# Optimization experiments

Hardware: AMD Instinct MI355X
Metric: run time of the kernel (lower is better)

## Reference

```python
import jax, jax.numpy as jnp
import numpy as np

B, CH, IMG, P = 16, 3, 384, 16
D, HEADS, DH, MLP, DEPTH = 384, 6, 64, 1536, 6
INNER = HEADS * DH
PD = P * P * 5 * CH          # SPT patch dim = 3840
GRID = IMG // P              # 24
NP = GRID * GRID             # 576 patches
SEQ = NP + 1                 # +cls = 577


def layer_norm(x, g, b, eps=1e-5):
    mu = jnp.mean(x, axis=-1, keepdims=True)
    var = jnp.var(x, axis=-1, keepdims=True)
    return (x - mu) * jax.lax.rsqrt(var + eps) * g + b


def spt_shifts(x):
    # F.pad semantics: (left,right,top,bottom) with negative = crop
    s1 = jnp.pad(x, ((0, 0), (0, 0), (0, 0), (1, 0)))[:, :, :, :-1]  # (1,-1,0,0)
    s2 = jnp.pad(x, ((0, 0), (0, 0), (0, 0), (0, 1)))[:, :, :, 1:]   # (-1,1,0,0)
    s3 = jnp.pad(x, ((0, 0), (0, 0), (1, 0), (0, 0)))[:, :, :-1, :]  # (0,0,1,-1)
    s4 = jnp.pad(x, ((0, 0), (0, 0), (0, 1), (0, 0)))[:, :, 1:, :]   # (0,0,-1,1)
    return jnp.concatenate([x, s1, s2, s3, s4], axis=1)  # [b, 5c, H, W]


def patchify(x):
    # 'b c (h p1) (w p2) -> b (h w) (p1 p2 c)'
    b, c, _, _ = x.shape
    x = x.reshape(b, c, GRID, P, GRID, P)
    x = x.transpose(0, 2, 4, 3, 5, 1)  # b h w p1 p2 c
    return x.reshape(b, GRID * GRID, P * P * c)


def setup_inputs():
    key = jax.random.key(0)
    ks = jax.random.split(key, 16)
    img = jax.random.normal(ks[0], (B, CH, IMG, IMG), jnp.float32)
    spt_g = jnp.ones((PD,), jnp.float32)
    spt_b = jnp.zeros((PD,), jnp.float32)
    spt_w = jax.random.normal(ks[1], (PD, D), jnp.float32) * (1.0 / np.sqrt(PD))
    spt_bias = jnp.zeros((D,), jnp.float32)
    pos = jax.random.normal(ks[2], (1, SEQ, D), jnp.float32) * 0.02
    cls = jax.random.normal(ks[3], (1, 1, D), jnp.float32) * 0.02
    attn_g = jnp.ones((DEPTH, D), jnp.float32)
    attn_b = jnp.zeros((DEPTH, D), jnp.float32)
    temp = jnp.full((DEPTH,), np.log(DH ** -0.5), jnp.float32)
    wqkv = jax.random.normal(ks[4], (DEPTH, D, 3 * INNER), jnp.float32) * 0.02
    wout = jax.random.normal(ks[5], (DEPTH, INNER, D), jnp.float32) * 0.02
    bout = jnp.zeros((DEPTH, D), jnp.float32)
    ff_g = jnp.ones((DEPTH, D), jnp.float32)
    ff_b = jnp.zeros((DEPTH, D), jnp.float32)
    w1 = jax.random.normal(ks[6], (DEPTH, D, MLP), jnp.float32) * 0.02
    b1 = jnp.zeros((DEPTH, MLP), jnp.float32)
    w2 = jax.random.normal(ks[7], (DEPTH, MLP, D), jnp.float32) * 0.02
    b2 = jnp.zeros((DEPTH, D), jnp.float32)
    return {"img": img, "spt_g": spt_g, "spt_b": spt_b, "spt_w": spt_w,
            "spt_bias": spt_bias, "pos": pos, "cls": cls, "attn_g": attn_g,
            "attn_b": attn_b, "temp": temp, "wqkv": wqkv, "wout": wout,
            "bout": bout, "ff_g": ff_g, "ff_b": ff_b, "w1": w1, "b1": b1,
            "w2": w2, "b2": b2}


def vit_forward(img, spt_g, spt_b, spt_w, spt_bias, pos, cls, attn_g, attn_b,
                temp, wqkv, wout, bout, ff_g, ff_b, w1, b1, w2, b2):
    # SPT patch embedding
    x = patchify(spt_shifts(img))                      # [b, NP, PD]
    x = layer_norm(x, spt_g, spt_b) @ spt_w + spt_bias  # [b, NP, D]
    b = x.shape[0]
    cls_tok = jnp.broadcast_to(cls, (b, 1, D))
    x = jnp.concatenate([cls_tok, x], axis=1) + pos[:, :SEQ]

    eye = jnp.eye(SEQ, dtype=bool)
    neg = -jnp.finfo(x.dtype).max

    def block(x, p):
        ag, ab, t, wq, wo, bo, fg, fb, W1, B1, W2, B2 = p
        h = layer_norm(x, ag, ab)
        qkv = h @ wq                                   # [b, n, 3*inner]
        q, k, v = jnp.split(qkv, 3, axis=-1)
        q = q.reshape(b, SEQ, HEADS, DH).transpose(0, 2, 1, 3)
        k = k.reshape(b, SEQ, HEADS, DH).transpose(0, 2, 1, 3)
        v = v.reshape(b, SEQ, HEADS, DH).transpose(0, 2, 1, 3)
        dots = jnp.einsum('bhid,bhjd->bhij', q, k) * jnp.exp(t)
        dots = jnp.where(eye, neg, dots)               # diagonal mask (LSA)
        attn = jax.nn.softmax(dots, axis=-1)
        out = jnp.einsum('bhij,bhjd->bhid', attn, v)
        out = out.transpose(0, 2, 1, 3).reshape(b, SEQ, INNER)
        x = out @ wo + bo + x
        h = layer_norm(x, fg, fb)
        x = jax.nn.gelu(h @ W1 + B1, approximate=False) @ W2 + B2 + x
        return x, None

    params = (attn_g, attn_b, temp, wqkv, wout, bout, ff_g, ff_b, w1, b1, w2, b2)
    x, _ = jax.lax.scan(block, x, params)
    return x


def reference(img, spt_g, spt_b, spt_w, spt_bias, pos, cls, attn_g, attn_b,
              temp, wqkv, wout, bout, ff_g, ff_b, w1, b1, w2, b2):
    return vit_forward(img, spt_g, spt_b, spt_w, spt_bias, pos, cls, attn_g,
                       attn_b, temp, wqkv, wout, bout, ff_g, ff_b, w1, b1,
                       w2, b2)
```

## Files before the change

kernel.cpp:

```cpp
#include <hip/hip_runtime.h>

typedef unsigned short ushort_t;
typedef __bf16 bf16x8 __attribute__((ext_vector_type(8)));
typedef float f32x4 __attribute__((ext_vector_type(4)));

#define SEQ_ 577
#define D_ 384
#define NTOK (16 * 577)

enum { M_QKV = 0, M_OUT, M_MLP1, M_MLP2 };

__device__ inline float b2f(ushort_t u) {
    unsigned int x = ((unsigned int)u) << 16;
    float f; __builtin_memcpy(&f, &x, 4); return f;
}
__device__ inline ushort_t f2b(float f) {
    unsigned int x; __builtin_memcpy(&x, &f, 4);
    x = x + 0x7fffu + ((x >> 16) & 1u);
    return (ushort_t)(x >> 16);
}

__device__ void transpose_tile(const float* __restrict__ src,
                               ushort_t* __restrict__ dst,
                               int ldn, int ldk, int k0, int n0)
{
    __shared__ float t[64][65];
    const int tid = threadIdx.x;
    const int c = tid & 63, rr = tid >> 6;
#pragma unroll
    for (int i = 0; i < 16; i++) {
        int kl = rr + i * 4;
        t[kl][c] = src[(size_t)(k0 + kl) * ldn + n0 + c];
    }
    __syncthreads();
#pragma unroll
    for (int i = 0; i < 16; i++) {
        int nl = rr + i * 4;
        dst[(size_t)(n0 + nl) * ldk + k0 + c] = f2b(t[c][nl]);
    }
}

__global__ __launch_bounds__(256) void prep_spt_kernel(
    const float* __restrict__ w, ushort_t* __restrict__ wt)
{
    transpose_tile(w, wt, 384, 3840, blockIdx.x * 64, blockIdx.y * 64);
}

__global__ __launch_bounds__(256) void prep_all_kernel(
    const float* __restrict__ wqkv, const float* __restrict__ wout,
    const float* __restrict__ w1, const float* __restrict__ w2,
    ushort_t* __restrict__ W6)
{
    int id = blockIdx.x;
    int l = id / 432;
    int r = id - l * 432;
    ushort_t* qkv_t  = W6 + (size_t)l * 1769472;
    ushort_t* wout_t = qkv_t + 442368;
    ushort_t* w1_t   = wout_t + 147456;
    ushort_t* w2_t   = w1_t + 589824;
    const float* wq = wqkv + (size_t)l * 442368;
    const float* wo = wout + (size_t)l * 147456;
    const float* W1 = w1 + (size_t)l * 589824;
    const float* W2 = w2 + (size_t)l * 589824;
    if (r < 108) {
        int kt = r / 18, nt = r % 18;
        transpose_tile(wq, qkv_t, 1152, 384, kt * 64, nt * 64);
    } else if (r < 144) {
        r -= 108; int kt = r / 6, nt = r % 6;
        transpose_tile(wo, wout_t, 384, 384, kt * 64, nt * 64);
    } else if (r < 288) {
        r -= 144; int kt = r / 24, nt = r % 24;
        transpose_tile(W1, w1_t, 1536, 384, kt * 64, nt * 64);
    } else {
        r -= 288; int kt = r / 6, nt = r % 6;
        transpose_tile(W2, w2_t, 384, 1536, kt * 64, nt * 64);
    }
}

template <int MODE>
__global__ __launch_bounds__(256) void gemm64(
    const ushort_t* __restrict__ A, const ushort_t* __restrict__ Bt,
    ushort_t* __restrict__ Co, float* __restrict__ resid,
    const float* __restrict__ bias,
    int M, int K, int ldc)
{
    __shared__ __align__(16) ushort_t As[2][64][40];
    __shared__ __align__(16) ushort_t Bs[2][64][40];

    const int gx = gridDim.x;
    const int nwg = gx * gridDim.y;
    const int f = blockIdx.y * gx + blockIdx.x;
    const int q = nwg >> 3, rr_ = nwg & 7;
    const int xcd = f & 7, ii = f >> 3;
    const int swz = (xcd < rr_ ? xcd * (q + 1) : rr_ * (q + 1) + (xcd - rr_) * q) + ii;
    const int bx = swz % gx, by = swz / gx;

    const int tid = threadIdx.x;
    const int rowBase = by * 64;
    const int colBase = bx * 64;
    const int nk = K >> 5;
    const int lr = tid >> 2, lk = (tid & 3) * 8;
    const int wv = tid >> 6, lane = tid & 63;
    const int wm = (wv >> 1) * 32, wn = (wv & 1) * 32;
    const int m16 = lane & 15, q4 = lane >> 4, kb = q4 * 8;

    const ushort_t* pa = A + (size_t)(rowBase + lr) * K + lk;
    const ushort_t* pb = Bt + (size_t)(colBase + lr) * K + lk;

    f32x4 acc[2][2];
#pragma unroll
    for (int i = 0; i < 2; i++)
#pragma unroll
        for (int j = 0; j < 2; j++) acc[i][j] = (f32x4){0.f, 0.f, 0.f, 0.f};

    uint4 Ua, Ub, Va, Vb;
    auto gloadU = [&](int kt) {
        Ua = *(const uint4*)(pa + kt * 32);
        Ub = *(const uint4*)(pb + kt * 32);
    };
    auto gloadV = [&](int kt) {
        Va = *(const uint4*)(pa + kt * 32);
        Vb = *(const uint4*)(pb + kt * 32);
    };
    auto swriteU = [&](int buf) {
        *(uint4*)&As[buf][lr][lk] = Ua;
        *(uint4*)&Bs[buf][lr][lk] = Ub;
    };
    auto swriteV = [&](int buf) {
        *(uint4*)&As[buf][lr][lk] = Va;
        *(uint4*)&Bs[buf][lr][lk] = Vb;
    };
    auto compute = [&](int buf) {
        bf16x8 a0 = *(const bf16x8*)&As[buf][wm + m16][kb];
        bf16x8 a1 = *(const bf16x8*)&As[buf][wm + 16 + m16][kb];
        bf16x8 b0 = *(const bf16x8*)&Bs[buf][wn + m16][kb];
        bf16x8 b1 = *(const bf16x8*)&Bs[buf][wn + 16 + m16][kb];
        acc[0][0] = __builtin_amdgcn_mfma_f32_16x16x32_bf16(a0, b0, acc[0][0], 0, 0, 0);
        acc[0][1] = __builtin_amdgcn_mfma_f32_16x16x32_bf16(a0, b1, acc[0][1], 0, 0, 0);
        acc[1][0] = __builtin_amdgcn_mfma_f32_16x16x32_bf16(a1, b0, acc[1][0], 0, 0, 0);
        acc[1][1] = __builtin_amdgcn_mfma_f32_16x16x32_bf16(a1, b1, acc[1][1], 0, 0, 0);
    };

    gloadU(0);
    swriteU(0);
    gloadU(1);
    gloadV(2);
    __syncthreads();

    for (int kt = 0; kt < nk; kt += 2) {
        swriteU(1);
        if (kt + 3 < nk) gloadU(kt + 3);
        compute(0);
        __syncthreads();
        if (kt + 2 < nk) {
            swriteV(0);
            if (kt + 4 < nk) gloadV(kt + 4);
        }
        compute(1);
        __syncthreads();
    }

#pragma unroll
    for (int im = 0; im < 2; im++)
#pragma unroll
        for (int in = 0; in < 2; in++) {
            int col = colBase + wn + in * 16 + m16;
#pragma unroll
            for (int r = 0; r < 4; r++) {
                int row = rowBase + wm + im * 16 + q4 * 4 + r;
                if (row >= M) continue;
                float v = acc[im][in][r];
                if (MODE == M_QKV) {
                    Co[(size_t)row * ldc + col] = f2b(v);
                } else if (MODE == M_MLP1) {
                    float t = v + bias[col];
                    float u = t * (0.7978845608f + 0.0356774081f * t * t);
                    float e = __builtin_amdgcn_exp2f(2.885390082f * u);
                    float gl = t - t * __builtin_amdgcn_rcpf(e + 1.0f);
                    Co[(size_t)row * ldc + col] = f2b(gl);
                } else {
                    size_t o = (size_t)row * ldc + col;
                    resid[o] = resid[o] + v + bias[col];
                }
            }
        }
}

__global__ __launch_bounds__(256) void gemm64_spt_split(
    const ushort_t* __restrict__ A, const ushort_t* __restrict__ Bt,
    float* __restrict__ resid, int rowOff)
{
    __shared__ __align__(16) ushort_t As[2][64][40];
    __shared__ __align__(16) ushort_t Bs[2][64][40];

    const int f = blockIdx.z * 288 + blockIdx.y * 6 + blockIdx.x;
    const int swz = (f & 7) * 144 + (f >> 3);
    const int bz = swz / 288;
    const int rem = swz - bz * 288;
    const int by = rem / 6, bx = rem - by * 6;

    const int K = 3840, nk = 30;
    const int rowBase = by * 64;
    const int colBase = bx * 64;
    const int kbase = bz * 960;

    const int tid = threadIdx.x;
    const int lr = tid >> 2, lk = (tid & 3) * 8;
    const int wv = tid >> 6, lane = tid & 63;
    const int wm = (wv >> 1) * 32, wn = (wv & 1) * 32;
    const int m16 = lane & 15, q4 = lane >> 4, kb = q4 * 8;

    const ushort_t* pa = A + (size_t)(rowBase + lr) * K + kbase + lk;
    const ushort_t* pb = Bt + (size_t)(colBase + lr) * K + kbase + lk;

    f32x4 acc[2][2];
#pragma unroll
    for (int i = 0; i < 2; i++)
#pragma unroll
        for (int j = 0; j < 2; j++) acc[i][j] = (f32x4){0.f, 0.f, 0.f, 0.f};

    uint4 Ua, Ub, Va, Vb;
    auto gloadU = [&](int kt) {
        Ua = *(const uint4*)(pa + kt * 32);
        Ub = *(const uint4*)(pb + kt * 32);
    };
    auto gloadV = [&](int kt) {
        Va = *(const uint4*)(pa + kt * 32);
        Vb = *(const uint4*)(pb + kt * 32);
    };
    auto swriteU = [&](int buf) {
        *(uint4*)&As[buf][lr][lk] = Ua;
        *(uint4*)&Bs[buf][lr][lk] = Ub;
    };
    auto swriteV = [&](int buf) {
        *(uint4*)&As[buf][lr][lk] = Va;
        *(uint4*)&Bs[buf][lr][lk] = Vb;
    };
    auto compute = [&](int buf) {
        bf16x8 a0 = *(const bf16x8*)&As[buf][wm + m16][kb];
        bf16x8 a1 = *(const bf16x8*)&As[buf][wm + 16 + m16][kb];
        bf16x8 b0 = *(const bf16x8*)&Bs[buf][wn + m16][kb];
        bf16x8 b1 = *(const bf16x8*)&Bs[buf][wn + 16 + m16][kb];
        acc[0][0] = __builtin_amdgcn_mfma_f32_16x16x32_bf16(a0, b0, acc[0][0], 0, 0, 0);
        acc[0][1] = __builtin_amdgcn_mfma_f32_16x16x32_bf16(a0, b1, acc[0][1], 0, 0, 0);
        acc[1][0] = __builtin_amdgcn_mfma_f32_16x16x32_bf16(a1, b0, acc[1][0], 0, 0, 0);
        acc[1][1] = __builtin_amdgcn_mfma_f32_16x16x32_bf16(a1, b1, acc[1][1], 0, 0, 0);
    };

    gloadU(0);
    swriteU(0);
    gloadU(1);
    gloadV(2);
    __syncthreads();

    for (int kt = 0; kt < nk; kt += 2) {
        swriteU(1);
        if (kt + 3 < nk) gloadU(kt + 3);
        compute(0);
        __syncthreads();
        if (kt + 2 < nk) {
            swriteV(0);
            if (kt + 4 < nk) gloadV(kt + 4);
        }
        compute(1);
        __syncthreads();
    }

#pragma unroll
    for (int im = 0; im < 2; im++)
#pragma unroll
        for (int in = 0; in < 2; in++) {
            int col = colBase + wn + in * 16 + m16;
#pragma unroll
            for (int r = 0; r < 4; r++) {
                int row = rowBase + wm + im * 16 + q4 * 4 + r;
                int grow = rowOff + row;
                int bb = grow / 576, p = grow - bb * 576;
                size_t o = ((size_t)(bb * SEQ_ + 1 + p)) * D_ + col;
                atomicAdd(&resid[o], acc[im][in][r]);
            }
        }
}

__global__ __launch_bounds__(256) void attn_kernel(
    const ushort_t* __restrict__ qkv, ushort_t* __restrict__ attn,
    const float* __restrict__ temp, int layer)
{
    const int qt = blockIdx.x;
    const int bh = blockIdx.y;
    const int b = bh / 6, hd = bh - b * 6;
    const int tid = threadIdx.x;
    const int wv = tid >> 6, lane = tid & 63;
    const int m16 = lane & 15, q4 = lane >> 4;
    const float sc2 = expf(temp[layer]) * 1.44269504f;

    __shared__ __align__(16) ushort_t Ks[64][72];
    __shared__ __align__(16) ushort_t Vt[64][72];
    __shared__ __align__(16) ushort_t Pw[4][16][72];

    const int qrow = qt * 64 + wv * 16 + m16;
    const int qtok = qrow < SEQ_ ? qrow : SEQ_ - 1;
    const ushort_t* qb = qkv + ((size_t)(b * SEQ_ + qtok)) * 1152 + hd * 64;
    bf16x8 qf0 = *(const bf16x8*)(qb + q4 * 8);
    bf16x8 qf1 = *(const bf16x8*)(qb + 32 + q4 * 8);

    f32x4 accO[4];
#pragma unroll
    for (int dt = 0; dt < 4; dt++) accO[dt] = (f32x4){0.f, 0.f, 0.f, 0.f};
    float l_r[4] = {0.f, 0.f, 0.f, 0.f};

    const int skey = tid >> 2;
    const int scol = (tid & 3) * 16;
    const int vp   = tid & 31;
    const int vdh  = (tid >> 5) * 8;

    for (int kt = 0; kt < 10; kt++) {
        int key = kt * 64 + skey;
        int gkey = key < SEQ_ ? key : 0;
        const ushort_t* kb_ = qkv + ((size_t)(b * SEQ_ + gkey)) * 1152 + 384 + hd * 64;
        uint4 kv0 = *(const uint4*)(kb_ + scol);
        uint4 kv1 = *(const uint4*)(kb_ + scol + 8);
        if (key >= SEQ_) { kv0 = (uint4){0, 0, 0, 0}; kv1 = kv0; }
        int vk0 = kt * 64 + 2 * vp;
        int t0 = vk0 < SEQ_ ? vk0 : 0;
        int t1 = vk0 + 1 < SEQ_ ? vk0 + 1 : 0;
        uint4 va = *(const uint4*)(qkv + ((size_t)(b * SEQ_ + t0)) * 1152 + 768 + hd * 64 + vdh);
        uint4 vb2 = *(const uint4*)(qkv + ((size_t)(b * SEQ_ + t1)) * 1152 + 768 + hd * 64 + vdh);
        if (vk0 >= SEQ_) va = (uint4){0, 0, 0, 0};
        if (vk0 + 1 >= SEQ_) vb2 = (uint4){0, 0, 0, 0};
        __syncthreads();
        *(uint4*)&Ks[skey][scol] = kv0;
        *(uint4*)&Ks[skey][scol + 8] = kv1;
        {
            const ushort_t* e0 = (const ushort_t*)&va;
            const ushort_t* e1 = (const ushort_t*)&vb2;
#pragma unroll
            for (int j = 0; j < 8; j++) {
                unsigned int pack = (unsigned int)e0[j] | ((unsigned int)e1[j] << 16);
                *(unsigned int*)&Vt[vdh + j][2 * vp] = pack;
            }
        }
        __syncthreads();

        f32x4 s[4];
#pragma unroll
        for (int ct = 0; ct < 4; ct++) {
            bf16x8 b0 = *(const bf16x8*)&Ks[ct * 16 + m16][q4 * 8];
            bf16x8 b1 = *(const bf16x8*)&Ks[ct * 16 + m16][32 + q4 * 8];
            f32x4 z = (f32x4){0.f, 0.f, 0.f, 0.f};
            z = __builtin_amdgcn_mfma_f32_16x16x32_bf16(qf0, b0, z, 0, 0, 0);
            z = __builtin_amdgcn_mfma_f32_16x16x32_bf16(qf1, b1, z, 0, 0, 0);
            s[ct] = z;
        }
        const int rowb = qt * 64 + wv * 16 + q4 * 4;
#pragma unroll
        for (int r = 0; r < 4; r++) {
            float rs = 0.f;
#pragma unroll
            for (int ct = 0; ct < 4; ct++) {
                int col = kt * 64 + ct * 16 + m16;
                float v = s[ct][r] * sc2;
                if (col >= SEQ_ || col == rowb + r) v = -1.0e30f;
                float p = __builtin_amdgcn_exp2f(v);
                s[ct][r] = p;
                rs += p;
            }
            rs += __shfl_xor(rs, 1);
            rs += __shfl_xor(rs, 2);
            rs += __shfl_xor(rs, 4);
            rs += __shfl_xor(rs, 8);
            l_r[r] += rs;
        }
#pragma unroll
        for (int ct = 0; ct < 4; ct++)
#pragma unroll
            for (int r = 0; r < 4; r++)
                Pw[wv][q4 * 4 + r][ct * 16 + m16] = f2b(s[ct][r]);
        bf16x8 pf0 = *(const bf16x8*)&Pw[wv][m16][q4 * 8];
        bf16x8 pf1 = *(const bf16x8*)&Pw[wv][m16][32 + q4 * 8];
#pragma unroll
        for (int dt = 0; dt < 4; dt++) {
            bf16x8 vb0 = *(const bf16x8*)&Vt[dt * 16 + m16][q4 * 8];
            bf16x8 vb1 = *(const bf16x8*)&Vt[dt * 16 + m16][32 + q4 * 8];
            f32x4 o = accO[dt];
            o = __builtin_amdgcn_mfma_f32_16x16x32_bf16(pf0, vb0, o, 0, 0, 0);
            o = __builtin_amdgcn_mfma_f32_16x16x32_bf16(pf1, vb1, o, 0, 0, 0);
            accO[dt] = o;
        }
    }

    const int rowb = qt * 64 + wv * 16 + q4 * 4;
#pragma unroll
    for (int r = 0; r < 4; r++) {
        int grow = rowb + r;
        if (grow >= SEQ_) continue;
        float inv = 1.f / l_r[r];
        ushort_t* op = attn + ((size_t)(b * SEQ_ + grow)) * 384 + hd * 64;
#pragma unroll
        for (int dt = 0; dt < 4; dt++)
            op[dt * 16 + m16] = f2b(accO[dt][r] * inv);
    }
}

__global__ __launch_bounds__(256) void spt_ln_kernel(
    const float* __restrict__ img, const float* __restrict__ gg,
    const float* __restrict__ bb_, ushort_t* __restrict__ Xn, int r0)
{
    int bp = r0 + blockIdx.x;
    int b = bp / 576, p = bp - b * 576;
    int ph = p / 24, pw = p - ph * 24;

    __shared__ float vals[3840];
    __shared__ float red[10];

    const int tid = threadIdx.x;
    const int p1 = tid >> 4, p2 = tid & 15;

    float s = 0.f, sq = 0.f;
#pragma unroll
    for (int plane = 0; plane < 15; plane++) {
        int g5 = plane / 3, ch = plane - g5 * 3;
        int row = ph * 16 + p1, col = pw * 16 + p2;
        if (g5 == 1) col -= 1;
        else if (g5 == 2) col += 1;
        else if (g5 == 3) row -= 1;
        else if (g5 == 4) row += 1;
        float v = 0.f;
        if (row >= 0 && row < 384 && col >= 0 && col < 384)
            v = img[((size_t)(b * 3 + ch) * 384 + row) * 384 + col];
        vals[tid * 15 + plane] = v;
        s += v; sq += v * v;
    }
#pragma unroll
    for (int off = 32; off > 0; off >>= 1) {
        s += __shfl_xor(s, off);
        sq += __shfl_xor(sq, off);
    }
    int wid = tid >> 6;
    if ((tid & 63) == 0) { red[wid] = s; red[4 + wid] = sq; }
    __syncthreads();
    if (tid == 0) {
        float S = red[0] + red[1] + red[2] + red[3];
        float Q = red[4] + red[5] + red[6] + red[7];
        float mean = S / 3840.f;
        float var = Q / 3840.f - mean * mean;
        red[8] = mean;
        red[9] = rsqrtf(var + 1e-5f);
    }
    __syncthreads();
    float mean = red[8], rstd = red[9];
#pragma unroll
    for (int i = 0; i < 15; i++) {
        int k = tid + i * 256;
        float v = (vals[k] - mean) * rstd * gg[k] + bb_[k];
        Xn[(size_t)blockIdx.x * 3840 + k] = f2b(v);
    }
}

__global__ __launch_bounds__(256) void ln_kernel(
    const float* __restrict__ x, const float* __restrict__ g,
    const float* __restrict__ b, ushort_t* __restrict__ h)
{
    int row = blockIdx.x * 4 + (threadIdx.x >> 6);
    int lane = threadIdx.x & 63;
    const float4* xr = (const float4*)(x + (size_t)row * 384);
    float4 a = xr[lane];
    float4 c = (lane < 32) ? xr[64 + lane] : make_float4(0.f, 0.f, 0.f, 0.f);
    float s = a.x + a.y + a.z + a.w + c.x + c.y + c.z + c.w;
    float sq = a.x * a.x + a.y * a.y + a.z * a.z + a.w * a.w
             + c.x * c.x + c.y * c.y + c.z * c.z + c.w * c.w;
#pragma unroll
    for (int off = 32; off > 0; off >>= 1) {
        s += __shfl_xor(s, off);
        sq += __shfl_xor(sq, off);
    }
    float mean = s / 384.f;
    float var = sq / 384.f - mean * mean;
    float rstd = rsqrtf(var + 1e-5f);
    const float4* g4 = (const float4*)g;
    const float4* b4 = (const float4*)b;
    ushort_t* hr = h + (size_t)row * 384;
    {
        float4 gv = g4[lane], bv = b4[lane];
        unsigned int lo = (unsigned int)f2b((a.x - mean) * rstd * gv.x + bv.x)
                        | ((unsigned int)f2b((a.y - mean) * rstd * gv.y + bv.y) << 16);
        unsigned int hi = (unsigned int)f2b((a.z - mean) * rstd * gv.z + bv.z)
                        | ((unsigned int)f2b((a.w - mean) * rstd * gv.w + bv.w) << 16);
        *(uint2*)&hr[lane * 4] = make_uint2(lo, hi);
    }
    if (lane < 32) {
        float4 gv = g4[64 + lane], bv = b4[64 + lane];
        unsigned int lo = (unsigned int)f2b((c.x - mean) * rstd * gv.x + bv.x)
                        | ((unsigned int)f2b((c.y - mean) * rstd * gv.y + bv.y) << 16);
        unsigned int hi = (unsigned int)f2b((c.z - mean) * rstd * gv.z + bv.z)
                        | ((unsigned int)f2b((c.w - mean) * rstd * gv.w + bv.w) << 16);
        *(uint2*)&hr[256 + lane * 4] = make_uint2(lo, hi);
    }
}

__global__ void init_x_kernel(const float* __restrict__ cls,
                              const float* __restrict__ pos,
                              const float* __restrict__ spt_bias,
                              float* __restrict__ x)
{
    int s = blockIdx.x, b = blockIdx.y, d = threadIdx.x;
    float base = (s == 0) ? cls[d] : spt_bias[d];
    x[((size_t)b * SEQ_ + s) * D_ + d] = base + pos[(size_t)s * D_ + d];
}

extern "C" void kernel_launch(void* const* d_in, const int* in_sizes, int n_in,
                              void* d_out, int out_size, void* d_ws, size_t ws_size,
                              hipStream_t stream)
{
    const float* img      = (const float*)d_in[0];
    const float* spt_g    = (const float*)d_in[1];
    const float* spt_b    = (const float*)d_in[2];
    const float* spt_w    = (const float*)d_in[3];
    const float* spt_bias = (const float*)d_in[4];
    const float* pos      = (const float*)d_in[5];
    const float* clsp     = (const float*)d_in[6];
    const float* attn_g   = (const float*)d_in[7];
    const float* attn_b   = (const float*)d_in[8];
    const float* temp     = (const float*)d_in[9];
    const float* wqkv     = (const float*)d_in[10];
    const float* wout     = (const float*)d_in[11];
    const float* bout     = (const float*)d_in[12];
    const float* ff_g     = (const float*)d_in[13];
    const float* ff_b     = (const float*)d_in[14];
    const float* w1       = (const float*)d_in[15];
    const float* b1       = (const float*)d_in[16];
    const float* w2       = (const float*)d_in[17];
    const float* b2       = (const float*)d_in[18];

    float* x = (float*)d_out;

    char* base = (char*)d_ws;
    ushort_t* qkv   = (ushort_t*)base;
    ushort_t* attn  = (ushort_t*)(base + (size_t)NTOK * 1152 * 2);
    ushort_t* Xn    = (ushort_t*)base;
    ushort_t* gbuf  = (ushort_t*)base;
    ushort_t* spt_wt = (ushort_t*)(base + 23592960);
    char* p2 = base + (size_t)NTOK * 1536 * 2;
    ushort_t* h  = (ushort_t*)p2;
    char* p3 = p2 + (size_t)NTOK * 384 * 2;
    ushort_t* W6 = (ushort_t*)p3;

    prep_all_kernel<<<2592, 256, 0, stream>>>(wqkv, wout, w1, w2, W6);
    prep_spt_kernel<<<dim3(60, 6), 256, 0, stream>>>(spt_w, spt_wt);
    init_x_kernel<<<dim3(SEQ_, 16), 384, 0, stream>>>(clsp, pos, spt_bias, x);

    for (int c = 0; c < 3; c++) {
        int r0 = c * 3072;
        spt_ln_kernel<<<3072, 256, 0, stream>>>(img, spt_g, spt_b, Xn, r0);
        gemm64_spt_split<<<dim3(6, 48, 4), 256, 0, stream>>>(Xn, spt_wt, x, r0);
    }

    for (int l = 0; l < 6; l++) {
        ushort_t* qkv_t  = W6 + (size_t)l * 1769472;
        ushort_t* wout_t = qkv_t + 442368;
        ushort_t* w1_t   = wout_t + 147456;
        ushort_t* w2_t   = w1_t + 589824;
        ln_kernel<<<NTOK / 4, 256, 0, stream>>>(x, attn_g + l * 384, attn_b + l * 384, h);
        gemm64<M_QKV><<<dim3(18, 145), 256, 0, stream>>>(
            h, qkv_t, qkv, nullptr, nullptr, NTOK, 384, 1152);
        attn_kernel<<<dim3(10, 96), 256, 0, stream>>>(qkv, attn, temp, l);
        gemm64<M_OUT><<<dim3(6, 145), 256, 0, stream>>>(
            attn, wout_t, nullptr, x, bout + l * 384, NTOK, 384, 384);
        ln_kernel<<<NTOK / 4, 256, 0, stream>>>(x, ff_g + l * 384, ff_b + l * 384, h);
        gemm64<M_MLP1><<<dim3(24, 145), 256, 0, stream>>>(
            h, w1_t, gbuf, nullptr, b1 + l * 1536, NTOK, 384, 1536);
        gemm64<M_MLP2><<<dim3(6, 145), 256, 0, stream>>>(
            gbuf, w2_t, nullptr, x, b2 + l * 384, NTOK, 1536, 384);
    }
}
```

Baseline: 1.200 ms.

## Replace LDS-staged GEMMs with direct-load MFMA, prefetch attention KV, merge prep kernels

The transformer GEMMs no longer stage tiles through shared memory. Each wave now loads its MFMA operands straight from global memory, with K fixed as a template parameter and the loop unrolled. This removes LDS writes and barriers, but each A/B element is loaded twice from global memory and now depends on cache hits. The attention kernel gains an XCD-aware block swizzle and register prefetch of the next K/V tile, and the SPT weight transpose is folded into the combined prep kernel launch.

```diff
diff --git a/kernel.cpp b/kernel.cpp
--- a/kernel.cpp
+++ b/kernel.cpp
@@ -40,18 +40,19 @@
     }
 }
 
-__global__ __launch_bounds__(256) void prep_spt_kernel(
-    const float* __restrict__ w, ushort_t* __restrict__ wt)
-{
-    transpose_tile(w, wt, 384, 3840, blockIdx.x * 64, blockIdx.y * 64);
-}
-
 __global__ __launch_bounds__(256) void prep_all_kernel(
     const float* __restrict__ wqkv, const float* __restrict__ wout,
     const float* __restrict__ w1, const float* __restrict__ w2,
-    ushort_t* __restrict__ W6)
+    const float* __restrict__ spt_w,
+    ushort_t* __restrict__ W6, ushort_t* __restrict__ spt_wt)
 {
     int id = blockIdx.x;
+    if (id >= 2592) {
+        int r2 = id - 2592;
+        int kt = r2 % 60, nt = r2 / 60;
+        transpose_tile(spt_w, spt_wt, 384, 3840, kt * 64, nt * 64);
+        return;
+    }
     int l = id / 432;
     int r = id - l * 432;
     ushort_t* qkv_t  = W6 + (size_t)l * 1769472;
@@ -77,15 +78,14 @@
     }
 }
 
-template <int MODE>
-__global__ __launch_bounds__(256) void gemm64(
+template <int MODE, int NK>
+__global__ __launch_bounds__(256) void gemm_direct(
     const ushort_t* __restrict__ A, const ushort_t* __restrict__ Bt,
     ushort_t* __restrict__ Co, float* __restrict__ resid,
     const float* __restrict__ bias,
-    int M, int K, int ldc)
-{
-    __shared__ __align__(16) ushort_t As[2][64][40];
-    __shared__ __align__(16) ushort_t Bs[2][64][40];
+    int M, int ldc)
+{
+    const int K = NK * 32;
 
     const int gx = gridDim.x;
     const int nwg = gx * gridDim.y;
@@ -95,17 +95,87 @@
     const int swz = (xcd < rr_ ? xcd * (q + 1) : rr_ * (q + 1) + (xcd - rr_) * q) + ii;
     const int bx = swz % gx, by = swz / gx;
 
-    const int tid = threadIdx.x;
     const int rowBase = by * 64;
     const int colBase = bx * 64;
-    const int nk = K >> 5;
+    const int lane = threadIdx.x & 63, wv = threadIdx.x >> 6;
+    const int wm = (wv >> 1) * 32, wn = (wv & 1) * 32;
+    const int m16 = lane & 15, q4 = lane >> 4;
+
+    const ushort_t* pa0 = A + (size_t)(rowBase + wm + m16) * K + q4 * 8;
+    const ushort_t* pa1 = pa0 + (size_t)16 * K;
+    const ushort_t* pb0 = Bt + (size_t)(colBase + wn + m16) * K + q4 * 8;
+    const ushort_t* pb1 = pb0 + (size_t)16 * K;
+
+    f32x4 acc[2][2];
+#pragma unroll
+    for (int i = 0; i < 2; i++)
+#pragma unroll
+        for (int j = 0; j < 2; j++) acc[i][j] = (f32x4){0.f, 0.f, 0.f, 0.f};
+
+#pragma unroll 4
+    for (int kt = 0; kt < NK; kt++) {
+        bf16x8 a0 = *(const bf16x8*)(pa0 + kt * 32);
+        bf16x8 a1 = *(const bf16x8*)(pa1 + kt * 32);
+        bf16x8 b0 = *(const bf16x8*)(pb0 + kt * 32);
+        bf16x8 b1 = *(const bf16x8*)(pb1 + kt * 32);
+        acc[0][0] = __builtin_amdgcn_mfma_f32_16x16x32_bf16(a0, b0, acc[0][0], 0, 0, 0);
+        acc[0][1] = __builtin_amdgcn_mfma_f32_16x16x32_bf16(a0, b1, acc[0][1], 0, 0, 0);
+        acc[1][0] = __builtin_amdgcn_mfma_f32_16x16x32_bf16(a1, b0, acc[1][0], 0, 0, 0);
+        acc[1][1] = __builtin_amdgcn_mfma_f32_16x16x32_bf16(a1, b1, acc[1][1], 0, 0, 0);
+    }
+
+#pragma unroll
+    for (int im = 0; im < 2; im++)
+#pragma unroll
+        for (int in = 0; in < 2; in++) {
+            int col = colBase + wn + in * 16 + m16;
+#pragma unroll
+            for (int r = 0; r < 4; r++) {
+                int row = rowBase + wm + im * 16 + q4 * 4 + r;
+                if (row >= M) continue;
+                float v = acc[im][in][r];
+                if (MODE == M_QKV) {
+                    Co[(size_t)row * ldc + col] = f2b(v);
+                } else if (MODE == M_MLP1) {
+                    float t = v + bias[col];
+                    float u = t * (0.7978845608f + 0.0356774081f * t * t);
+                    float e = __builtin_amdgcn_exp2f(2.885390082f * u);
+                    float gl = t - t * __builtin_amdgcn_rcpf(e + 1.0f);
+                    Co[(size_t)row * ldc + col] = f2b(gl);
+                } else {
+                    size_t o = (size_t)row * ldc + col;
+                    resid[o] = resid[o] + v + bias[col];
+                }
+            }
+        }
+}
+
+__global__ __launch_bounds__(256) void gemm64_spt_split(
+    const ushort_t* __restrict__ A, const ushort_t* __restrict__ Bt,
+    float* __restrict__ resid, int rowOff)
+{
+    __shared__ __align__(16) ushort_t As[2][64][40];
+    __shared__ __align__(16) ushort_t Bs[2][64][40];
+
+    const int f = blockIdx.z * 288 + blockIdx.y * 6 + blockIdx.x;
+    const int swz = (f & 7) * 144 + (f >> 3);
+    const int bz = swz / 288;
+    const int rem = swz - bz * 288;
+    const int by = rem / 6, bx = rem - by * 6;
+
+    const int K = 3840, nk = 30;
+    const int rowBase = by * 64;
+    const int colBase = bx * 64;
+    const int kbase = bz * 960;
+
+    const int tid = threadIdx.x;
     const int lr = tid >> 2, lk = (tid & 3) * 8;
     const int wv = tid >> 6, lane = tid & 63;
     const int wm = (wv >> 1) * 32, wn = (wv & 1) * 32;
     const int m16 = lane & 15, q4 = lane >> 4, kb = q4 * 8;
 
-    const ushort_t* pa = A + (size_t)(rowBase + lr) * K + lk;
-    const ushort_t* pb = Bt + (size_t)(colBase + lr) * K + lk;
+    const ushort_t* pa = A + (size_t)(rowBase + lr) * K + kbase + lk;
+    const ushort_t* pb = Bt + (size_t)(colBase + lr) * K + kbase + lk;
 
     f32x4 acc[2][2];
 #pragma unroll
@@ -168,112 +238,6 @@
 #pragma unroll
             for (int r = 0; r < 4; r++) {
                 int row = rowBase + wm + im * 16 + q4 * 4 + r;
-                if (row >= M) continue;
-                float v = acc[im][in][r];
-                if (MODE == M_QKV) {
-                    Co[(size_t)row * ldc + col] = f2b(v);
-                } else if (MODE == M_MLP1) {
-                    float t = v + bias[col];
-                    float u = t * (0.7978845608f + 0.0356774081f * t * t);
-                    float e = __builtin_amdgcn_exp2f(2.885390082f * u);
-                    float gl = t - t * __builtin_amdgcn_rcpf(e + 1.0f);
-                    Co[(size_t)row * ldc + col] = f2b(gl);
-                } else {
-                    size_t o = (size_t)row * ldc + col;
-                    resid[o] = resid[o] + v + bias[col];
-                }
-            }
-        }
-}
-
-__global__ __launch_bounds__(256) void gemm64_spt_split(
-    const ushort_t* __restrict__ A, const ushort_t* __restrict__ Bt,
-    float* __restrict__ resid, int rowOff)
-{
-    __shared__ __align__(16) ushort_t As[2][64][40];
-    __shared__ __align__(16) ushort_t Bs[2][64][40];
-
-    const int f = blockIdx.z * 288 + blockIdx.y * 6 + blockIdx.x;
-    const int swz = (f & 7) * 144 + (f >> 3);
-    const int bz = swz / 288;
-    const int rem = swz - bz * 288;
-    const int by = rem / 6, bx = rem - by * 6;
-
-    const int K = 3840, nk = 30;
-    const int rowBase = by * 64;
-    const int colBase = bx * 64;
-    const int kbase = bz * 960;
-
-    const int tid = threadIdx.x;
-    const int lr = tid >> 2, lk = (tid & 3) * 8;
-    const int wv = tid >> 6, lane = tid & 63;
-    const int wm = (wv >> 1) * 32, wn = (wv & 1) * 32;
-    const int m16 = lane & 15, q4 = lane >> 4, kb = q4 * 8;
-
-    const ushort_t* pa = A + (size_t)(rowBase + lr) * K + kbase + lk;
-    const ushort_t* pb = Bt + (size_t)(colBase + lr) * K + kbase + lk;
-
-    f32x4 acc[2][2];
-#pragma unroll
-    for (int i = 0; i < 2; i++)
-#pragma unroll
-        for (int j = 0; j < 2; j++) acc[i][j] = (f32x4){0.f, 0.f, 0.f, 0.f};
-
-    uint4 Ua, Ub, Va, Vb;
-    auto gloadU = [&](int kt) {
-        Ua = *(const uint4*)(pa + kt * 32);
-        Ub = *(const uint4*)(pb + kt * 32);
-    };
-    auto gloadV = [&](int kt) {
-        Va = *(const uint4*)(pa + kt * 32);
-        Vb = *(const uint4*)(pb + kt * 32);
-    };
-    auto swriteU = [&](int buf) {
-        *(uint4*)&As[buf][lr][lk] = Ua;
-        *(uint4*)&Bs[buf][lr][lk] = Ub;
-    };
-    auto swriteV = [&](int buf) {
-        *(uint4*)&As[buf][lr][lk] = Va;
-        *(uint4*)&Bs[buf][lr][lk] = Vb;
-    };
-    auto compute = [&](int buf) {
-        bf16x8 a0 = *(const bf16x8*)&As[buf][wm + m16][kb];
-        bf16x8 a1 = *(const bf16x8*)&As[buf][wm + 16 + m16][kb];
-        bf16x8 b0 = *(const bf16x8*)&Bs[buf][wn + m16][kb];
-        bf16x8 b1 = *(const bf16x8*)&Bs[buf][wn + 16 + m16][kb];
-        acc[0][0] = __builtin_amdgcn_mfma_f32_16x16x32_bf16(a0, b0, acc[0][0], 0, 0, 0);
-        acc[0][1] = __builtin_amdgcn_mfma_f32_16x16x32_bf16(a0, b1, acc[0][1], 0, 0, 0);
-        acc[1][0] = __builtin_amdgcn_mfma_f32_16x16x32_bf16(a1, b0, acc[1][0], 0, 0, 0);
-        acc[1][1] = __builtin_amdgcn_mfma_f32_16x16x32_bf16(a1, b1, acc[1][1], 0, 0, 0);
-    };
-
-    gloadU(0);
-    swriteU(0);
-    gloadU(1);
-    gloadV(2);
-    __syncthreads();
-
-    for (int kt = 0; kt < nk; kt += 2) {
-        swriteU(1);
-        if (kt + 3 < nk) gloadU(kt + 3);
-        compute(0);
-        __syncthreads();
-        if (kt + 2 < nk) {
-            swriteV(0);
-            if (kt + 4 < nk) gloadV(kt + 4);
-        }
-        compute(1);
-        __syncthreads();
-    }
-
-#pragma unroll
-    for (int im = 0; im < 2; im++)
-#pragma unroll
-        for (int in = 0; in < 2; in++) {
-            int col = colBase + wn + in * 16 + m16;
-#pragma unroll
-            for (int r = 0; r < 4; r++) {
-                int row = rowBase + wm + im * 16 + q4 * 4 + r;
                 int grow = rowOff + row;
                 int bb = grow / 576, p = grow - bb * 576;
                 size_t o = ((size_t)(bb * SEQ_ + 1 + p)) * D_ + col;
@@ -286,8 +250,10 @@
     const ushort_t* __restrict__ qkv, ushort_t* __restrict__ attn,
     const float* __restrict__ temp, int layer)
 {
-    const int qt = blockIdx.x;
-    const int bh = blockIdx.y;
+    const int f = blockIdx.y * 10 + blockIdx.x;
+    const int swz = (f & 7) * 120 + (f >> 3);
+    const int qt = swz % 10;
+    const int bh = swz / 10;
     const int b = bh / 6, hd = bh - b * 6;
     const int tid = threadIdx.x;
     const int wv = tid >> 6, lane = tid & 63;
@@ -314,20 +280,26 @@
     const int vp   = tid & 31;
     const int vdh  = (tid >> 5) * 8;
 
-    for (int kt = 0; kt < 10; kt++) {
+    uint4 kv0, kv1, va, vb2;
+    auto loadKV = [&](int kt) {
         int key = kt * 64 + skey;
         int gkey = key < SEQ_ ? key : 0;
         const ushort_t* kb_ = qkv + ((size_t)(b * SEQ_ + gkey)) * 1152 + 384 + hd * 64;
-        uint4 kv0 = *(const uint4*)(kb_ + scol);
-        uint4 kv1 = *(const uint4*)(kb_ + scol + 8);
+        kv0 = *(const uint4*)(kb_ + scol);
+        kv1 = *(const uint4*)(kb_ + scol + 8);
         if (key >= SEQ_) { kv0 = (uint4){0, 0, 0, 0}; kv1 = kv0; }
         int vk0 = kt * 64 + 2 * vp;
         int t0 = vk0 < SEQ_ ? vk0 : 0;
         int t1 = vk0 + 1 < SEQ_ ? vk0 + 1 : 0;
-        uint4 va = *(const uint4*)(qkv + ((size_t)(b * SEQ_ + t0)) * 1152 + 768 + hd * 64 + vdh);
-        uint4 vb2 = *(const uint4*)(qkv + ((size_t)(b * SEQ_ + t1)) * 1152 + 768 + hd * 64 + vdh);
+        va  = *(const uint4*)(qkv + ((size_t)(b * SEQ_ + t0)) * 1152 + 768 + hd * 64 + vdh);
+        vb2 = *(const uint4*)(qkv + ((size_t)(b * SEQ_ + t1)) * 1152 + 768 + hd * 64 + vdh);
         if (vk0 >= SEQ_) va = (uint4){0, 0, 0, 0};
         if (vk0 + 1 >= SEQ_) vb2 = (uint4){0, 0, 0, 0};
+    };
+
+    loadKV(0);
+
+    for (int kt = 0; kt < 10; kt++) {
         __syncthreads();
         *(uint4*)&Ks[skey][scol] = kv0;
         *(uint4*)&Ks[skey][scol + 8] = kv1;
@@ -341,6 +313,7 @@
             }
         }
         __syncthreads();
+        if (kt + 1 < 10) loadKV(kt + 1);
 
         f32x4 s[4];
 #pragma unroll
@@ -545,8 +518,7 @@
     char* p3 = p2 + (size_t)NTOK * 384 * 2;
     ushort_t* W6 = (ushort_t*)p3;
 
-    prep_all_kernel<<<2592, 256, 0, stream>>>(wqkv, wout, w1, w2, W6);
-    prep_spt_kernel<<<dim3(60, 6), 256, 0, stream>>>(spt_w, spt_wt);
+    prep_all_kernel<<<2952, 256, 0, stream>>>(wqkv, wout, w1, w2, spt_w, W6, spt_wt);
     init_x_kernel<<<dim3(SEQ_, 16), 384, 0, stream>>>(clsp, pos, spt_bias, x);
 
     for (int c = 0; c < 3; c++) {
@@ -561,15 +533,15 @@
         ushort_t* w1_t   = wout_t + 147456;
         ushort_t* w2_t   = w1_t + 589824;
         ln_kernel<<<NTOK / 4, 256, 0, stream>>>(x, attn_g + l * 384, attn_b + l * 384, h);
-        gemm64<M_QKV><<<dim3(18, 145), 256, 0, stream>>>(
-            h, qkv_t, qkv, nullptr, nullptr, NTOK, 384, 1152);
+        gemm_direct<M_QKV, 12><<<dim3(18, 145), 256, 0, stream>>>(
+            h, qkv_t, qkv, nullptr, nullptr, NTOK, 1152);
         attn_kernel<<<dim3(10, 96), 256, 0, stream>>>(qkv, attn, temp, l);
-        gemm64<M_OUT><<<dim3(6, 145), 256, 0, stream>>>(
-            attn, wout_t, nullptr, x, bout + l * 384, NTOK, 384, 384);
+        gemm_direct<M_OUT, 12><<<dim3(6, 145), 256, 0, stream>>>(
+            attn, wout_t, nullptr, x, bout + l * 384, NTOK, 384);
         ln_kernel<<<NTOK / 4, 256, 0, stream>>>(x, ff_g + l * 384, ff_b + l * 384, h);
-        gemm64<M_MLP1><<<dim3(24, 145), 256, 0, stream>>>(
-            h, w1_t, gbuf, nullptr, b1 + l * 1536, NTOK, 384, 1536);
-        gemm64<M_MLP2><<<dim3(6, 145), 256, 0, stream>>>(
-            gbuf, w2_t, nullptr, x, b2 + l * 384, NTOK, 1536, 384);
-    }
-}
+        gemm_direct<M_MLP1, 12><<<dim3(24, 145), 256, 0, stream>>>(
+            h, w1_t, gbuf, nullptr, b1 + l * 1536, NTOK, 1536);
+        gemm_direct<M_MLP2, 48><<<dim3(6, 145), 256, 0, stream>>>(
+            gbuf, w2_t, nullptr, x, b2 + l * 384, NTOK, 384);
+    }
+}
```

New measurement: 2.133 ms. 1.78x slower.
